# Optimization experiments

Measured on AMD Instinct MI355X. Metric: run time of the kernel, lower is better.

The kernel has to match this reference:

```python
import jax, jax.numpy as jnp
import numpy as np

B, M = 128, 1024
D_Z, D_PHI = 1024, 512
H1, H2 = 512, 512


def setup_inputs() -> dict:
    key = jax.random.key(0)
    ks = jax.random.split(key, 8)
    s1 = 1.0 / np.sqrt(D_Z + D_PHI)
    s2 = 1.0 / np.sqrt(H1)
    s3 = 1.0 / np.sqrt(H2)
    return {
        "g_q": jax.random.normal(ks[0], (B, D_Z), jnp.float32),
        "Phi": jax.random.normal(ks[1], (M, D_PHI), jnp.float32),
        "W1": jax.random.normal(ks[2], (D_Z + D_PHI, H1), jnp.float32) * s1,
        "b1": jnp.zeros((H1,), jnp.float32),
        "W2": jax.random.normal(ks[3], (H1, H2), jnp.float32) * s2,
        "b2": jnp.zeros((H2,), jnp.float32),
        "W3": jax.random.normal(ks[4], (H2, 1), jnp.float32) * s3,
        "b3": jnp.zeros((1,), jnp.float32),
    }


def reference(g_q, Phi, W1, b1, W2, b2, W3, b3):
    # net(cat([z_exp, phi_exp])) == (g_q @ W1[:d_z]) broadcast-summed with
    # (Phi @ W1[d_z:]) -- identical math, avoids materializing [B, M, d_z+d_phi].
    d_z = g_q.shape[1]
    hz = g_q @ W1[:d_z]          # [B, H1]
    hp = Phi @ W1[d_z:]          # [M, H1]
    h = hz[:, None, :] + hp[None, :, :] + b1      # [B, M, H1]
    h = jax.nn.gelu(h, approximate=False)         # torch GELU is exact erf form
    h = jax.nn.gelu(h @ W2 + b2, approximate=False)  # [B, M, H2]
    u = h @ W3 + b3                                # [B, M, 1]
    return u[..., 0]                               # [B, M]
```

## Files before the change

kernel.cpp:

```cpp
#include <hip/hip_runtime.h>
#include <hip/hip_bf16.h>


typedef __bf16 bf16x8 __attribute__((ext_vector_type(8)));
typedef float  f32x4  __attribute__((ext_vector_type(4)));
typedef float  f32x2  __attribute__((ext_vector_type(2)));

__device__ __forceinline__ f32x2 gelu_pk(f32x2 x) {
    f32x2 t = x * x;
    f32x2 p = __builtin_elementwise_fma(t, f32x2{0.1029436f, 0.1029436f},
                                        f32x2{2.3022082f, 2.3022082f});
    f32x2 a = p * x;
    f32x2 e;
    e.x = __builtin_amdgcn_exp2f(a.x);
    e.y = __builtin_amdgcn_exp2f(a.y);
    f32x2 d = e + f32x2{1.f, 1.f};
    f32x2 r;
    r.x = __builtin_amdgcn_rcpf(d.x);
    r.y = __builtin_amdgcn_rcpf(d.y);
    return __builtin_elementwise_fma(-x, r, x);
}

__device__ __forceinline__ unsigned int pack_bf16x2(float a, float b) {
    __hip_bfloat162 h = __float22bfloat162_rn(make_float2(a, b));
    return *reinterpret_cast<unsigned int*>(&h);
}
__device__ __forceinline__ float bf_lo(unsigned int u) {
    return __builtin_bit_cast(float, u << 16);
}
__device__ __forceinline__ float bf_hi(unsigned int u) {
    return __builtin_bit_cast(float, u & 0xffff0000u);
}

__global__ __launch_bounds__(256) void wcast_kernel(
    const float* __restrict__ W1, const float* __restrict__ W2,
    unsigned short* __restrict__ W1F, unsigned short* __restrict__ W2F)
{
    __shared__ float tr[64 * 68];
    const int t = threadIdx.x;
    const int id = blockIdx.x;

    const float* src;
    unsigned short* dst;
    int kt, nt;
    if (id < 64) { src = W2; dst = W2F; kt = id >> 3; nt = id & 7; }
    else         { src = W1; dst = W1F; kt = (id - 64) >> 3; nt = (id - 64) & 7; }
    const int k0 = kt * 64, n0 = nt * 64;

    {
        int r = t >> 2, c16 = (t & 3) * 16;
        #pragma unroll
        for (int q = 0; q < 4; ++q)
            *(float4*)&tr[r * 68 + c16 + q * 4] =
                *(const float4*)&src[(k0 + r) * 512 + n0 + c16 + q * 4];
    }
    __syncthreads();
    const int nl = t >> 2, kc16 = (t & 3) * 16;
    unsigned int pk[8];
    #pragma unroll
    for (int i = 0; i < 8; ++i) {
        float f0 = tr[(kc16 + 2 * i    ) * 68 + nl];
        float f1 = tr[(kc16 + 2 * i + 1) * 68 + nl];
        pk[i] = pack_bf16x2(f0, f1);
    }
    const int n  = n0 + nl;
    const int nf = n >> 4;
    #pragma unroll
    for (int h = 0; h < 2; ++h) {
        int kbase = k0 + kc16 + h * 8;
        int kc = kbase >> 5;
        int k8 = (kbase >> 3) & 3;
        int lane = (n & 15) + 16 * k8;
        uint4 v = h ? make_uint4(pk[4], pk[5], pk[6], pk[7])
                    : make_uint4(pk[0], pk[1], pk[2], pk[3]);
        *(uint4*)&dst[(unsigned)((kc * 32 + nf) * 512 + lane * 8)] = v;
    }
}

__global__ __launch_bounds__(512) void l1_kernel(
    const float* __restrict__ g_q, const float* __restrict__ Phi,
    const unsigned short* __restrict__ W1F, const float* __restrict__ b1,
    float* __restrict__ hzb, unsigned short* __restrict__ hpb)
{
    __shared__ __align__(16) unsigned short lA[64 * 64];

    const int t = threadIdx.x;
    const int w = t >> 6;
    const int l = t & 63;
    const int bi = blockIdx.x;
    const bool is_hz = bi < 2;
    const int r0 = is_hz ? bi * 64 : (bi - 2) * 64;
    const int ld = is_hz ? 1024 : 512;
    const int nkt = is_hz ? 16 : 8;
    const int kcb = is_hz ? 0 : 32;
    const float* src = is_hz ? g_q : Phi;

    f32x4 acc[4][4];
    #pragma unroll
    for (int a = 0; a < 4; ++a)
        #pragma unroll
        for (int bf = 0; bf < 4; ++bf)
            acc[a][bf] = f32x4{0.f, 0.f, 0.f, 0.f};

    const int arow = t >> 3;
    const int ac   = t & 7;
    const float* srow = src + (unsigned)(r0 + arow) * ld;
    const unsigned int awoff = (unsigned)(arow * 128 + ((ac ^ (arow & 7)) << 4));

    #pragma unroll 1
    for (int kt = 0; kt < nkt; ++kt) {
        uint4 breg[2][4];
        #pragma unroll
        for (int kk = 0; kk < 2; ++kk)
            #pragma unroll
            for (int bf = 0; bf < 4; ++bf)
                breg[kk][bf] = *(const uint4*)
                    &W1F[(unsigned)(((kcb + kt * 2 + kk) * 32 + w * 4 + bf) * 512 + l * 8)];

        {
            float4 p0 = *(const float4*)&srow[kt * 64 + ac * 8];
            float4 p1 = *(const float4*)&srow[kt * 64 + ac * 8 + 4];
            uint4 pk;
            pk.x = pack_bf16x2(p0.x, p0.y);
            pk.y = pack_bf16x2(p0.z, p0.w);
            pk.z = pack_bf16x2(p1.x, p1.y);
            pk.w = pack_bf16x2(p1.z, p1.w);
            *(uint4*)((char*)lA + awoff) = pk;
        }
        __syncthreads();

        #pragma unroll
        for (int kk = 0; kk < 2; ++kk) {
            const int cch = kk * 4 + (l >> 4);
            bf16x8 af[4];
            #pragma unroll
            for (int a = 0; a < 4; ++a) {
                int row = 16 * a + (l & 15);
                unsigned off = (unsigned)(row * 128 + ((cch ^ (row & 7)) << 4));
                af[a] = __builtin_bit_cast(bf16x8, *(const uint4*)((const char*)lA + off));
            }
            #pragma unroll
            for (int bf = 0; bf < 4; ++bf) {
                bf16x8 bfr = __builtin_bit_cast(bf16x8, breg[kk][bf]);
                #pragma unroll
                for (int a = 0; a < 4; ++a)
                    acc[a][bf] = __builtin_amdgcn_mfma_f32_16x16x32_bf16(
                        af[a], bfr, acc[a][bf], 0, 0, 0);
            }
        }
        __syncthreads();
    }

    const int cl = l & 15, rq = (l >> 4) * 4;
    #pragma unroll
    for (int bf = 0; bf < 4; ++bf) {
        int n = w * 64 + 16 * bf + cl;
        if (is_hz) {
            float bb = b1[n];
            #pragma unroll
            for (int a = 0; a < 4; ++a)
                #pragma unroll
                for (int r = 0; r < 4; ++r)
                    hzb[(unsigned)(r0 + 16 * a + rq + r) * 512 + n] = acc[a][bf][r] + bb;
        } else {
            #pragma unroll
            for (int a = 0; a < 4; ++a)
                #pragma unroll
                for (int r = 0; r < 4; ++r) {
                    __hip_bfloat16 v = __float2bfloat16(acc[a][bf][r]);
                    hpb[(unsigned)(r0 + 16 * a + rq + r) * 512 + n] =
                        *reinterpret_cast<unsigned short*>(&v);
                }
        }
    }
}

__global__ __launch_bounds__(512, 2) void fused_kernel(
    const float* __restrict__ hzb, const unsigned short* __restrict__ hpb,
    const unsigned short* __restrict__ W2F,
    const float* __restrict__ b2, const float* __restrict__ W3,
    const float* __restrict__ b3, float* __restrict__ out)
{
    __shared__ __align__(16) unsigned short lA[2 * 64 * 64];
    __shared__ __align__(16) unsigned short hstage[2 * 64 * 64];
    __shared__ __align__(16) float lhz[512];
    __shared__ float lred[8][64];

    const int t = threadIdx.x;
    const int w = __builtin_amdgcn_readfirstlane(t >> 6);
    const int l = t & 63;
    const int r0 = blockIdx.x * 64;
    const int b  = r0 >> 10;
    const int m0 = r0 & 1023;

    f32x4 acc[4][4];
    #pragma unroll
    for (int a = 0; a < 4; ++a)
        #pragma unroll
        for (int bf = 0; bf < 4; ++bf)
            acc[a][bf] = f32x4{0.f, 0.f, 0.f, 0.f};

    const int arow = t >> 3;
    const int ac   = t & 7;
    const unsigned short* hprow = hpb + (unsigned)(m0 + arow) * 512;
    const float4* lhz4 = (const float4*)lhz;
    const unsigned int awoff = (unsigned)(arow * 128 + ((ac ^ (arow & 7)) << 4));
    const unsigned int hoff  = (unsigned)(t * 16);

    auto HPSTAGE = [&](int kt, int buf) {
        __builtin_amdgcn_global_load_lds(
            (const __attribute__((address_space(1))) void*)(hprow + kt * 64 + ac * 8),
            (__attribute__((address_space(3))) void*)((char*)hstage + buf * 8192 + hoff),
            16, 0, 0);
    };

    auto AGEN = [&](int kt, int abuf) {
        uint4 hv = *(const uint4*)((const char*)hstage + (kt & 1) * 8192 + hoff);
        const int kb = kt * 64 + ac * 8;
        float4 z0 = lhz4[kb >> 2];
        float4 z1 = lhz4[(kb >> 2) + 1];
        f32x2 g0 = gelu_pk(f32x2{bf_lo(hv.x), bf_hi(hv.x)} + f32x2{z0.x, z0.y});
        f32x2 g1 = gelu_pk(f32x2{bf_lo(hv.y), bf_hi(hv.y)} + f32x2{z0.z, z0.w});
        f32x2 g2 = gelu_pk(f32x2{bf_lo(hv.z), bf_hi(hv.z)} + f32x2{z1.x, z1.y});
        f32x2 g3 = gelu_pk(f32x2{bf_lo(hv.w), bf_hi(hv.w)} + f32x2{z1.z, z1.w});
        uint4 pk;
        pk.x = pack_bf16x2(g0.x, g0.y);
        pk.y = pack_bf16x2(g1.x, g1.y);
        pk.z = pack_bf16x2(g2.x, g2.y);
        pk.w = pack_bf16x2(g3.x, g3.y);
        *(uint4*)((char*)lA + (unsigned)(abuf * 8192) + awoff) = pk;
    };

    HPSTAGE(0, 0);
    HPSTAGE(1, 1);
    lhz[t] = hzb[b * 512 + t];
    __syncthreads();
    AGEN(0, 0);
    __syncthreads();

    #pragma unroll 2
    for (int kt = 0; kt < 8; ++kt) {
        if (kt < 6) HPSTAGE(kt + 2, kt & 1);

        uint4 breg[2][4];
        #pragma unroll
        for (int kk = 0; kk < 2; ++kk)
            #pragma unroll
            for (int bf = 0; bf < 4; ++bf)
                breg[kk][bf] = *(const uint4*)
                    &W2F[(unsigned)(((kt * 2 + kk) * 32 + w * 4 + bf) * 512 + l * 8)];

        if (kt < 7) AGEN(kt + 1, (kt + 1) & 1);

        const char* abase = (const char*)lA + (kt & 1) * 8192;
        #pragma unroll
        for (int kk = 0; kk < 2; ++kk) {
            const int cch = kk * 4 + (l >> 4);
            bf16x8 af[4];
            #pragma unroll
            for (int a = 0; a < 4; ++a) {
                int row = 16 * a + (l & 15);
                unsigned off = (unsigned)(row * 128 + ((cch ^ (row & 7)) << 4));
                af[a] = __builtin_bit_cast(bf16x8, *(const uint4*)(abase + off));
            }
            #pragma unroll
            for (int bf = 0; bf < 4; ++bf) {
                bf16x8 bfr = __builtin_bit_cast(bf16x8, breg[kk][bf]);
                #pragma unroll
                for (int a = 0; a < 4; ++a)
                    acc[a][bf] = __builtin_amdgcn_mfma_f32_16x16x32_bf16(
                        af[a], bfr, acc[a][bf], 0, 0, 0);
            }
        }

        __syncthreads();
    }

    float b2v[4], w3v[4];
    #pragma unroll
    for (int bf = 0; bf < 4; ++bf) {
        int n = w * 64 + 16 * bf + (l & 15);
        b2v[bf] = b2[n];
        w3v[bf] = W3[n];
    }
    f32x2 ps[4][2];
    #pragma unroll
    for (int a = 0; a < 4; ++a) {
        ps[a][0] = f32x2{0.f, 0.f};
        ps[a][1] = f32x2{0.f, 0.f};
    }

    #pragma unroll
    for (int bf = 0; bf < 4; ++bf) {
        const f32x2 b2p = {b2v[bf], b2v[bf]};
        const f32x2 w3p = {w3v[bf], w3v[bf]};
        #pragma unroll
        for (int a = 0; a < 4; ++a) {
            f32x2 xlo = f32x2{acc[a][bf][0], acc[a][bf][1]} + b2p;
            f32x2 xhi = f32x2{acc[a][bf][2], acc[a][bf][3]} + b2p;
            ps[a][0] = __builtin_elementwise_fma(gelu_pk(xlo), w3p, ps[a][0]);
            ps[a][1] = __builtin_elementwise_fma(gelu_pk(xhi), w3p, ps[a][1]);
        }
    }

    float psum[4][4];
    #pragma unroll
    for (int a = 0; a < 4; ++a) {
        psum[a][0] = ps[a][0].x; psum[a][1] = ps[a][0].y;
        psum[a][2] = ps[a][1].x; psum[a][3] = ps[a][1].y;
    }

    #pragma unroll
    for (int a = 0; a < 4; ++a)
        #pragma unroll
        for (int r = 0; r < 4; ++r) {
            float v = psum[a][r];
            v += __shfl_xor(v, 1);
            v += __shfl_xor(v, 2);
            v += __shfl_xor(v, 4);
            v += __shfl_xor(v, 8);
            psum[a][r] = v;
        }

    if ((l & 15) == 0) {
        int gb = (l >> 4) * 4;
        #pragma unroll
        for (int a = 0; a < 4; ++a)
            #pragma unroll
            for (int r = 0; r < 4; ++r)
                lred[w][16 * a + gb + r] = psum[a][r];
    }
    __syncthreads();
    if (t < 64) {
        float s = b3[0];
        #pragma unroll
        for (int ww = 0; ww < 8; ++ww) s += lred[ww][t];
        out[r0 + t] = s;
    }
}

extern "C" void kernel_launch(void* const* d_in, const int* in_sizes, int n_in,
                              void* d_out, int out_size, void* d_ws, size_t ws_size,
                              hipStream_t stream) {
    (void)in_sizes; (void)n_in; (void)out_size; (void)ws_size;
    const float* g_q = (const float*)d_in[0];
    const float* Phi = (const float*)d_in[1];
    const float* W1  = (const float*)d_in[2];
    const float* b1  = (const float*)d_in[3];
    const float* W2  = (const float*)d_in[4];
    const float* b2  = (const float*)d_in[5];
    const float* W3  = (const float*)d_in[6];
    const float* b3  = (const float*)d_in[7];
    float* out = (float*)d_out;

    char* ws = (char*)d_ws;
    float*          hzb = (float*)ws;
    unsigned short* hpb = (unsigned short*)(ws + 262144);
    unsigned short* W2F = (unsigned short*)(ws + 1310720);
    unsigned short* W1F = (unsigned short*)(ws + 1835008);

    hipLaunchKernelGGL(wcast_kernel, dim3(256), dim3(256), 0, stream,
                       W1, W2, W1F, W2F);
    hipLaunchKernelGGL(l1_kernel, dim3(18), dim3(512), 0, stream,
                       g_q, Phi, W1F, b1, hzb, hpb);
    hipLaunchKernelGGL(fused_kernel, dim3(2048), dim3(512), 0, stream,
                       hzb, hpb, W2F, b2, W3, b3, out);
}
```

Measured before the change: 115.5 us.

## Move W2 cast into layer-1 kernel and split layer-1 tiles across more blocks

The W2 bf16 repacking moves out of the first weight-cast kernel and into the layer-1 GEMM launch, so it runs alongside the layer-1 work instead of before it. The layer-1 GEMM also drops from 512-thread blocks covering all 512 output columns to 256-thread blocks each covering 256 columns. That raises the block count from 18 to 36, plus 64 W2-cast blocks, to fill more compute units in these small prologue kernels. In exchange, each layer-1 block reloads its A tile once per column half, and the cast and GEMM blocks now share one kernel with divergent roles.

```diff
diff --git a/kernel.cpp b/kernel.cpp
--- a/kernel.cpp
+++ b/kernel.cpp
@@ -33,18 +33,12 @@
 }
 
 __global__ __launch_bounds__(256) void wcast_kernel(
-    const float* __restrict__ W1, const float* __restrict__ W2,
-    unsigned short* __restrict__ W1F, unsigned short* __restrict__ W2F)
+    const float* __restrict__ W1, unsigned short* __restrict__ W1F)
 {
     __shared__ float tr[64 * 68];
     const int t = threadIdx.x;
     const int id = blockIdx.x;
-
-    const float* src;
-    unsigned short* dst;
-    int kt, nt;
-    if (id < 64) { src = W2; dst = W2F; kt = id >> 3; nt = id & 7; }
-    else         { src = W1; dst = W1F; kt = (id - 64) >> 3; nt = (id - 64) & 7; }
+    const int kt = id >> 3, nt = id & 7;
     const int k0 = kt * 64, n0 = nt * 64;
 
     {
@@ -52,7 +46,7 @@
         #pragma unroll
         for (int q = 0; q < 4; ++q)
             *(float4*)&tr[r * 68 + c16 + q * 4] =
-                *(const float4*)&src[(k0 + r) * 512 + n0 + c16 + q * 4];
+                *(const float4*)&W1[(k0 + r) * 512 + n0 + c16 + q * 4];
     }
     __syncthreads();
     const int nl = t >> 2, kc16 = (t & 3) * 16;
@@ -73,104 +67,148 @@
         int lane = (n & 15) + 16 * k8;
         uint4 v = h ? make_uint4(pk[4], pk[5], pk[6], pk[7])
                     : make_uint4(pk[0], pk[1], pk[2], pk[3]);
-        *(uint4*)&dst[(unsigned)((kc * 32 + nf) * 512 + lane * 8)] = v;
-    }
-}
-
-__global__ __launch_bounds__(512) void l1_kernel(
+        *(uint4*)&W1F[(unsigned)((kc * 32 + nf) * 512 + lane * 8)] = v;
+    }
+}
+
+__global__ __launch_bounds__(256) void l1w2_kernel(
     const float* __restrict__ g_q, const float* __restrict__ Phi,
+    const float* __restrict__ W2,
     const unsigned short* __restrict__ W1F, const float* __restrict__ b1,
-    float* __restrict__ hzb, unsigned short* __restrict__ hpb)
+    float* __restrict__ hzb, unsigned short* __restrict__ hpb,
+    unsigned short* __restrict__ W2F)
 {
-    __shared__ __align__(16) unsigned short lA[64 * 64];
-
+    __shared__ __align__(16) float trf[64 * 68];
     const int t = threadIdx.x;
-    const int w = t >> 6;
-    const int l = t & 63;
-    const int bi = blockIdx.x;
-    const bool is_hz = bi < 2;
-    const int r0 = is_hz ? bi * 64 : (bi - 2) * 64;
-    const int ld = is_hz ? 1024 : 512;
-    const int nkt = is_hz ? 16 : 8;
-    const int kcb = is_hz ? 0 : 32;
-    const float* src = is_hz ? g_q : Phi;
-
-    f32x4 acc[4][4];
-    #pragma unroll
-    for (int a = 0; a < 4; ++a)
-        #pragma unroll
-        for (int bf = 0; bf < 4; ++bf)
-            acc[a][bf] = f32x4{0.f, 0.f, 0.f, 0.f};
-
-    const int arow = t >> 3;
-    const int ac   = t & 7;
-    const float* srow = src + (unsigned)(r0 + arow) * ld;
-    const unsigned int awoff = (unsigned)(arow * 128 + ((ac ^ (arow & 7)) << 4));
-
-    #pragma unroll 1
-    for (int kt = 0; kt < nkt; ++kt) {
-        uint4 breg[2][4];
-        #pragma unroll
-        for (int kk = 0; kk < 2; ++kk)
+    const int id = blockIdx.x;
+
+    if (id < 64) {
+        const int kt = id >> 3, nt = id & 7;
+        const int k0 = kt * 64, n0 = nt * 64;
+        {
+            int r = t >> 2, c16 = (t & 3) * 16;
+            #pragma unroll
+            for (int q = 0; q < 4; ++q)
+                *(float4*)&trf[r * 68 + c16 + q * 4] =
+                    *(const float4*)&W2[(k0 + r) * 512 + n0 + c16 + q * 4];
+        }
+        __syncthreads();
+        const int nl = t >> 2, kc16 = (t & 3) * 16;
+        unsigned int pk[8];
+        #pragma unroll
+        for (int i = 0; i < 8; ++i) {
+            float f0 = trf[(kc16 + 2 * i    ) * 68 + nl];
+            float f1 = trf[(kc16 + 2 * i + 1) * 68 + nl];
+            pk[i] = pack_bf16x2(f0, f1);
+        }
+        const int n  = n0 + nl;
+        const int nf = n >> 4;
+        #pragma unroll
+        for (int h = 0; h < 2; ++h) {
+            int kbase = k0 + kc16 + h * 8;
+            int kc = kbase >> 5;
+            int k8 = (kbase >> 3) & 3;
+            int lane = (n & 15) + 16 * k8;
+            uint4 v = h ? make_uint4(pk[4], pk[5], pk[6], pk[7])
+                        : make_uint4(pk[0], pk[1], pk[2], pk[3]);
+            *(uint4*)&W2F[(unsigned)((kc * 32 + nf) * 512 + lane * 8)] = v;
+        }
+    } else {
+        unsigned short* lA = (unsigned short*)trf;
+        const int bi = id - 64;
+        const bool is_hz = bi < 4;
+        int rt, ct;
+        if (is_hz) { rt = bi >> 1;        ct = bi & 1; }
+        else       { rt = (bi - 4) >> 1;  ct = (bi - 4) & 1; }
+        const int r0 = rt * 64, c0 = ct * 256;
+        const int ld = is_hz ? 1024 : 512;
+        const int nkt = is_hz ? 16 : 8;
+        const int kcb = is_hz ? 0 : 32;
+        const float* src = is_hz ? g_q : Phi;
+
+        const int w = t >> 6;
+        const int l = t & 63;
+
+        f32x4 acc[4][4];
+        #pragma unroll
+        for (int a = 0; a < 4; ++a)
             #pragma unroll
             for (int bf = 0; bf < 4; ++bf)
-                breg[kk][bf] = *(const uint4*)
-                    &W1F[(unsigned)(((kcb + kt * 2 + kk) * 32 + w * 4 + bf) * 512 + l * 8)];
-
-        {
-            float4 p0 = *(const float4*)&srow[kt * 64 + ac * 8];
-            float4 p1 = *(const float4*)&srow[kt * 64 + ac * 8 + 4];
-            uint4 pk;
-            pk.x = pack_bf16x2(p0.x, p0.y);
-            pk.y = pack_bf16x2(p0.z, p0.w);
-            pk.z = pack_bf16x2(p1.x, p1.y);
-            pk.w = pack_bf16x2(p1.z, p1.w);
-            *(uint4*)((char*)lA + awoff) = pk;
-        }
-        __syncthreads();
-
-        #pragma unroll
-        for (int kk = 0; kk < 2; ++kk) {
-            const int cch = kk * 4 + (l >> 4);
-            bf16x8 af[4];
-            #pragma unroll
-            for (int a = 0; a < 4; ++a) {
-                int row = 16 * a + (l & 15);
-                unsigned off = (unsigned)(row * 128 + ((cch ^ (row & 7)) << 4));
-                af[a] = __builtin_bit_cast(bf16x8, *(const uint4*)((const char*)lA + off));
+                acc[a][bf] = f32x4{0.f, 0.f, 0.f, 0.f};
+
+        #pragma unroll 1
+        for (int kt = 0; kt < nkt; ++kt) {
+            uint4 breg[2][4];
+            #pragma unroll
+            for (int kk = 0; kk < 2; ++kk)
+                #pragma unroll
+                for (int bf = 0; bf < 4; ++bf)
+                    breg[kk][bf] = *(const uint4*)
+                        &W1F[(unsigned)(((kcb + kt * 2 + kk) * 32 +
+                                         ct * 16 + w * 4 + bf) * 512 + l * 8)];
+
+            #pragma unroll
+            for (int h = 0; h < 2; ++h) {
+                int ci = h * 256 + t;
+                int arow = ci >> 3, ac = ci & 7;
+                const float* srow = src + (unsigned)(r0 + arow) * ld;
+                float4 p0 = *(const float4*)&srow[kt * 64 + ac * 8];
+                float4 p1 = *(const float4*)&srow[kt * 64 + ac * 8 + 4];
+                uint4 pk;
+                pk.x = pack_bf16x2(p0.x, p0.y);
+                pk.y = pack_bf16x2(p0.z, p0.w);
+                pk.z = pack_bf16x2(p1.x, p1.y);
+                pk.w = pack_bf16x2(p1.z, p1.w);
+                *(uint4*)((char*)lA +
+                          (unsigned)(arow * 128 + ((ac ^ (arow & 7)) << 4))) = pk;
             }
-            #pragma unroll
-            for (int bf = 0; bf < 4; ++bf) {
-                bf16x8 bfr = __builtin_bit_cast(bf16x8, breg[kk][bf]);
+            __syncthreads();
+
+            #pragma unroll
+            for (int kk = 0; kk < 2; ++kk) {
+                const int cch = kk * 4 + (l >> 4);
+                bf16x8 af[4];
+                #pragma unroll
+                for (int a = 0; a < 4; ++a) {
+                    int row = 16 * a + (l & 15);
+                    unsigned off = (unsigned)(row * 128 + ((cch ^ (row & 7)) << 4));
+                    af[a] = __builtin_bit_cast(bf16x8,
+                                *(const uint4*)((const char*)lA + off));
+                }
+                #pragma unroll
+                for (int bf = 0; bf < 4; ++bf) {
+                    bf16x8 bfr = __builtin_bit_cast(bf16x8, breg[kk][bf]);
+                    #pragma unroll
+                    for (int a = 0; a < 4; ++a)
+                        acc[a][bf] = __builtin_amdgcn_mfma_f32_16x16x32_bf16(
+                            af[a], bfr, acc[a][bf], 0, 0, 0);
+                }
+            }
+            __syncthreads();
+        }
+
+        const int cl = l & 15, rq = (l >> 4) * 4;
+        #pragma unroll
+        for (int bf = 0; bf < 4; ++bf) {
+            int n = c0 + w * 64 + 16 * bf + cl;
+            if (is_hz) {
+                float bb = b1[n];
                 #pragma unroll
                 for (int a = 0; a < 4; ++a)
-                    acc[a][bf] = __builtin_amdgcn_mfma_f32_16x16x32_bf16(
-                        af[a], bfr, acc[a][bf], 0, 0, 0);
+                    #pragma unroll
+                    for (int r = 0; r < 4; ++r)
+                        hzb[(unsigned)(r0 + 16 * a + rq + r) * 512 + n] =
+                            acc[a][bf][r] + bb;
+            } else {
+                #pragma unroll
+                for (int a = 0; a < 4; ++a)
+                    #pragma unroll
+                    for (int r = 0; r < 4; ++r) {
+                        __hip_bfloat16 v = __float2bfloat16(acc[a][bf][r]);
+                        hpb[(unsigned)(r0 + 16 * a + rq + r) * 512 + n] =
+                            *reinterpret_cast<unsigned short*>(&v);
+                    }
             }
-        }
-        __syncthreads();
-    }
-
-    const int cl = l & 15, rq = (l >> 4) * 4;
-    #pragma unroll
-    for (int bf = 0; bf < 4; ++bf) {
-        int n = w * 64 + 16 * bf + cl;
-        if (is_hz) {
-            float bb = b1[n];
-            #pragma unroll
-            for (int a = 0; a < 4; ++a)
-                #pragma unroll
-                for (int r = 0; r < 4; ++r)
-                    hzb[(unsigned)(r0 + 16 * a + rq + r) * 512 + n] = acc[a][bf][r] + bb;
-        } else {
-            #pragma unroll
-            for (int a = 0; a < 4; ++a)
-                #pragma unroll
-                for (int r = 0; r < 4; ++r) {
-                    __hip_bfloat16 v = __float2bfloat16(acc[a][bf][r]);
-                    hpb[(unsigned)(r0 + 16 * a + rq + r) * 512 + n] =
-                        *reinterpret_cast<unsigned short*>(&v);
-                }
         }
     }
 }
@@ -359,10 +397,10 @@
     unsigned short* W2F = (unsigned short*)(ws + 1310720);
     unsigned short* W1F = (unsigned short*)(ws + 1835008);
 
-    hipLaunchKernelGGL(wcast_kernel, dim3(256), dim3(256), 0, stream,
-                       W1, W2, W1F, W2F);
-    hipLaunchKernelGGL(l1_kernel, dim3(18), dim3(512), 0, stream,
-                       g_q, Phi, W1F, b1, hzb, hpb);
+    hipLaunchKernelGGL(wcast_kernel, dim3(192), dim3(256), 0, stream,
+                       W1, W1F);
+    hipLaunchKernelGGL(l1w2_kernel, dim3(100), dim3(256), 0, stream,
+                       g_q, Phi, W2, W1F, b1, hzb, hpb, W2F);
     hipLaunchKernelGGL(fused_kernel, dim3(2048), dim3(512), 0, stream,
                        hzb, hpb, W2F, b2, W3, b3, out);
 }
```

New measurement: 113.5 us. No clear change (-1.7%).
